# Kernel tuning notes

Measured on AMD Instinct MI355X. Metric: run time of the kernel, lower is better.

## Reference

```python
import jax, jax.numpy as jnp
import numpy as np

EPS = 1e-6

def _rmsnorm(x, w):
    # x: [..., Dh]
    inv = jax.lax.rsqrt(jnp.mean(x * x, axis=-1, keepdims=True) + EPS)
    return x * inv * w

def _apply_rope(x, rope):
    # x: [B, H, L, Dh], rope: [L, Dh//2, 2]
    L = x.shape[-2]
    cos = rope[:L, :, 0]  # [L, Dh//2]
    sin = rope[:L, :, 1]
    x_even = x[..., 0::2]
    x_odd = x[..., 1::2]
    rot = jnp.stack([x_even * cos - x_odd * sin,
                     x_even * sin + x_odd * cos], axis=-1)  # [B,H,L,Dh//2,2]
    return rot.reshape(*x.shape[:-1], -1)


def setup_inputs() -> dict:
    key = jax.random.key(0)
    ks = jax.random.split(key, 4)
    B, L, D = 2, 2048, 1024
    H, Dh = 16, 64
    x = jax.random.normal(ks[0], (B, L, D), dtype=jnp.float32)
    rope = jax.random.normal(ks[1], (L, Dh // 2, 2), dtype=jnp.float32)
    w_qkv = jax.random.normal(ks[2], (3 * D, D), dtype=jnp.float32) * (1.0 / np.sqrt(D))
    w_proj = jax.random.normal(ks[3], (D, D), dtype=jnp.float32) * (1.0 / np.sqrt(D))
    q_norm_w = jnp.ones((Dh,), dtype=jnp.float32)
    k_norm_w = jnp.ones((Dh,), dtype=jnp.float32)
    return {"x": x, "rope": rope, "w_qkv": w_qkv, "w_proj": w_proj,
            "q_norm_w": q_norm_w, "k_norm_w": k_norm_w}


def reference(x, rope, w_qkv, w_proj, q_norm_w, k_norm_w):
    B, L, D = x.shape
    H = 16
    Dh = D // H
    qkv = jnp.einsum('bld,ed->ble', x, w_qkv).reshape(B, L, 3, H, Dh)
    qkv = jnp.transpose(qkv, (2, 0, 3, 1, 4))  # [3, B, H, L, Dh]
    q, k, v = qkv[0], qkv[1], qkv[2]
    q = _rmsnorm(q, q_norm_w)
    k = _rmsnorm(k, k_norm_w)
    q = _apply_rope(q, rope)
    k = _apply_rope(k, rope)
    scale = 1.0 / np.sqrt(Dh)
    scores = jnp.einsum('bhqd,bhkd->bhqk', q, k) * scale
    attn = jax.nn.softmax(scores, axis=-1)
    out = jnp.einsum('bhqk,bhkd->bhqd', attn, v)  # [B,H,L,Dh]
    out = jnp.transpose(out, (0, 2, 1, 3)).reshape(B, L, D)
    return jnp.einsum('bld,ed->ble', out, w_proj)
```

## Files before the change

### kernel.cpp

```cpp
#include <hip/hip_runtime.h>

typedef unsigned short u16;
typedef unsigned int u32;
typedef __bf16 bf16x8 __attribute__((ext_vector_type(8)));
typedef float f32x4 __attribute__((ext_vector_type(4)));

#define L_SEQ 2048
#define NH 16
#define DH 64
#define D_MODEL 1024
#define ATT_SHIFT2 14.426950408889634f

__device__ __forceinline__ u16 f2bf(float f) {
  union { float f; u32 u; } v; v.f = f;
  u32 u = v.u;
  return (u16)((u + 0x7fffu + ((u >> 16) & 1u)) >> 16);
}
__device__ __forceinline__ float bf2f(u16 b) {
  union { u32 u; float f; } v; v.u = ((u32)b) << 16;
  return v.f;
}
__device__ __forceinline__ u32 pk2(float lo_val, float hi_val) {
  union { float f; u32 u; } a, b;
  a.f = hi_val; b.f = lo_val;
  return __builtin_amdgcn_perm(a.u + 0x8000u, b.u + 0x8000u, 0x07060302u);
}
__device__ __forceinline__ u32 pk2t(float lo_val, float hi_val) {
  union { float f; u32 u; } a, b;
  a.f = hi_val; b.f = lo_val;
  return __builtin_amdgcn_perm(a.u, b.u, 0x07060302u);
}
__device__ __forceinline__ bf16x8 ld8(const u16* p) {
  union { uint4 u; bf16x8 b; } v;
  v.u = *(const uint4*)p;
  return v.b;
}
__device__ __forceinline__ f32x4 fzero4() { f32x4 z = {0.f, 0.f, 0.f, 0.f}; return z; }

__device__ __forceinline__ float fexp2(float x) {
#if __has_builtin(__builtin_amdgcn_exp2f)
  return __builtin_amdgcn_exp2f(x);
#else
  return __expf(x * 0.6931471805599453f);
#endif
}

__device__ __forceinline__ void gll16(const u16* g, u16* l) {
  __builtin_amdgcn_global_load_lds((const __attribute__((address_space(1))) u32*)g,
                                   (__attribute__((address_space(3))) u32*)l, 16, 0, 0);
}

__global__ __launch_bounds__(256) void cvt_bf16(const float* __restrict__ src,
                                                u16* __restrict__ dst, int n4) {
  int i = blockIdx.x * 256 + threadIdx.x;
  if (i >= n4) return;
  float4 v = ((const float4*)src)[i];
  ushort4 o = make_ushort4(f2bf(v.x), f2bf(v.y), f2bf(v.z), f2bf(v.w));
  ((ushort4*)dst)[i] = o;
}

template <int BM, bool OUT_BF16>
__global__ __launch_bounds__(256) void gemm_bt(const u16* __restrict__ A,
                                               const u16* __restrict__ B,
                                               void* __restrict__ Cp,
                                               int N, int K) {
  constexpr int MI = BM / 32;
  __shared__ u16 As[BM * 64];
  __shared__ u16 Bs[128 * 64];
  const int t = threadIdx.x;
  const int lane = t & 63, wv = t >> 6;
  const int col = lane & 15, quad = lane >> 4;
  const int wr = wv >> 1, wc = wv & 1;
  const int m0 = blockIdx.y * BM, n0 = blockIdx.x * 128;

  f32x4 acc[MI][4];
#pragma unroll
  for (int i = 0; i < MI; ++i)
#pragma unroll
    for (int j = 0; j < 4; ++j) acc[i][j] = fzero4();

  for (int kt = 0; kt < K; kt += 64) {
    __syncthreads();
#pragma unroll
    for (int it = 0; it < BM / 32; ++it) {
      int id0 = it * 256 + wv * 64;
      int id = id0 + lane;
      int row = id >> 3, cs = id & 7;
      int csrc = cs ^ (row & 7);
      gll16(A + (size_t)(m0 + row) * K + kt + csrc * 8, As + (size_t)id0 * 8);
    }
#pragma unroll
    for (int it = 0; it < 4; ++it) {
      int id0 = it * 256 + wv * 64;
      int id = id0 + lane;
      int row = id >> 3, cs = id & 7;
      int csrc = cs ^ (row & 7);
      gll16(B + (size_t)(n0 + row) * K + kt + csrc * 8, Bs + (size_t)id0 * 8);
    }
    __syncthreads();
#pragma unroll
    for (int c = 0; c < 2; ++c) {
      bf16x8 af[MI], bfv[4];
#pragma unroll
      for (int f = 0; f < MI; ++f) {
        int r = wr * (BM / 2) + f * 16 + col;
        af[f] = ld8(&As[(r * 8 + ((c * 4 + quad) ^ (r & 7))) * 8]);
      }
#pragma unroll
      for (int f = 0; f < 4; ++f) {
        int rb = wc * 64 + f * 16 + col;
        bfv[f] = ld8(&Bs[(rb * 8 + ((c * 4 + quad) ^ (rb & 7))) * 8]);
      }
#pragma unroll
      for (int i = 0; i < MI; ++i)
#pragma unroll
        for (int j = 0; j < 4; ++j)
          acc[i][j] = __builtin_amdgcn_mfma_f32_16x16x32_bf16(af[i], bfv[j], acc[i][j], 0, 0, 0);
    }
  }
#pragma unroll
  for (int i = 0; i < MI; ++i) {
    int gr = m0 + wr * (BM / 2) + i * 16 + quad * 4;
#pragma unroll
    for (int j = 0; j < 4; ++j) {
      int gc = n0 + wc * 64 + j * 16 + col;
#pragma unroll
      for (int r = 0; r < 4; ++r) {
        if (OUT_BF16)
          ((u16*)Cp)[(size_t)(gr + r) * N + gc] = f2bf(acc[i][j][r]);
        else
          ((float*)Cp)[(size_t)(gr + r) * N + gc] = acc[i][j][r];
      }
    }
  }
}

__global__ __launch_bounds__(256) void qk_norm_rope(const u16* __restrict__ qkvb,
                                                    const float* __restrict__ rope,
                                                    const float* __restrict__ qw,
                                                    const float* __restrict__ kw,
                                                    u16* __restrict__ qb,
                                                    u16* __restrict__ kb) {
  const int t = threadIdx.x;
  const int lane = t & 63, wv = t >> 6;
  const int gid = blockIdx.x * 4 + wv;
  const int l = gid & (L_SEQ - 1);
  const int b = gid >> 11;
  const int lg = lane & 7;
  const u16* base = qkvb + (size_t)gid * 3072 + lane * 8;
  const float QSCALE = 0.125f * 1.4426950408889634f;

  float wqv[8], wkv[8], rp[8];
  {
    float4 a = *(const float4*)(qw + lg * 8);
    float4 c = *(const float4*)(qw + lg * 8 + 4);
    wqv[0]=a.x; wqv[1]=a.y; wqv[2]=a.z; wqv[3]=a.w; wqv[4]=c.x; wqv[5]=c.y; wqv[6]=c.z; wqv[7]=c.w;
    a = *(const float4*)(kw + lg * 8);
    c = *(const float4*)(kw + lg * 8 + 4);
    wkv[0]=a.x; wkv[1]=a.y; wkv[2]=a.z; wkv[3]=a.w; wkv[4]=c.x; wkv[5]=c.y; wkv[6]=c.z; wkv[7]=c.w;
    a = *(const float4*)(rope + (size_t)l * 64 + lg * 8);
    c = *(const float4*)(rope + (size_t)l * 64 + lg * 8 + 4);
    rp[0]=a.x; rp[1]=a.y; rp[2]=a.z; rp[3]=a.w; rp[4]=c.x; rp[5]=c.y; rp[6]=c.z; rp[7]=c.w;
  }

#pragma unroll
  for (int i = 0; i < 2; ++i) {
    bf16x8 q8 = ld8(base + i * 512);
    bf16x8 k8 = ld8(base + 1024 + i * 512);
    float q[8], k[8];
#pragma unroll
    for (int j = 0; j < 8; ++j) { q[j] = (float)q8[j]; k[j] = (float)k8[j]; }
    float sq = 0.f, sk = 0.f;
#pragma unroll
    for (int j = 0; j < 8; ++j) { sq += q[j] * q[j]; sk += k[j] * k[j]; }
    sq += __shfl_xor(sq, 1); sq += __shfl_xor(sq, 2); sq += __shfl_xor(sq, 4);
    sk += __shfl_xor(sk, 1); sk += __shfl_xor(sk, 2); sk += __shfl_xor(sk, 4);
    float qi = rsqrtf(sq * (1.f / 64.f) + 1e-6f);
    float ki = rsqrtf(sk * (1.f / 64.f) + 1e-6f);

    float rq[8], rk[8];
#pragma unroll
    for (int j = 0; j < 4; ++j) {
      float cs = rp[2 * j], sn = rp[2 * j + 1];
      float qe = q[2 * j] * qi * wqv[2 * j], qo = q[2 * j + 1] * qi * wqv[2 * j + 1];
      float ke = k[2 * j] * ki * wkv[2 * j], ko = k[2 * j + 1] * ki * wkv[2 * j + 1];
      rq[2 * j]     = (qe * cs - qo * sn) * QSCALE;
      rq[2 * j + 1] = (qe * sn + qo * cs) * QSCALE;
      rk[2 * j]     = ke * cs - ko * sn;
      rk[2 * j + 1] = ke * sn + ko * cs;
    }
    uint4 qp = make_uint4(pk2(rq[0], rq[1]), pk2(rq[2], rq[3]), pk2(rq[4], rq[5]), pk2(rq[6], rq[7]));
    uint4 kp = make_uint4(pk2(rk[0], rk[1]), pk2(rk[2], rk[3]), pk2(rk[4], rk[5]), pk2(rk[6], rk[7]));
    const int head = (lane >> 3) + i * 8;
    size_t oi = (((size_t)(b * NH + head) * L_SEQ + l) * DH) + lg * 8;
    *(uint4*)(qb + oi) = qp;
    *(uint4*)(kb + oi) = kp;
  }
}

__global__ __launch_bounds__(256) void v_transpose(const u16* __restrict__ qkvb,
                                                   u16* __restrict__ vtb) {
  __shared__ u16 ldsT[64 * 64];
  const int t = threadIdx.x;
  const int bid = blockIdx.x;
  const int bh = bid >> 5;
  const int lt = (bid & 31) * 64;
  const int b = bh >> 4, h = bh & 15;
  const u16* src = qkvb + (size_t)(b * L_SEQ + lt) * 3072 + 2048 + h * 64;
#pragma unroll
  for (int i = 0; i < 2; ++i) {
    int idx = i * 256 + t;
    int ll = idx >> 3, dc = idx & 7;
    uint4 v = *(const uint4*)(src + (size_t)ll * 3072 + dc * 8);
    union { uint4 u; u16 s[8]; } vv; vv.u = v;
#pragma unroll
    for (int j = 0; j < 8; ++j) {
      int dh = dc * 8 + j;
      ldsT[dh * 64 + ((((ll >> 3) ^ (dh >> 3)) & 7) * 8 + (ll & 7))] = vv.s[j];
    }
  }
  __syncthreads();
#pragma unroll
  for (int i = 0; i < 2; ++i) {
    int idx = i * 256 + t;
    int dh = idx >> 3, lc = idx & 7;
    uint4 v = *(const uint4*)&ldsT[dh * 64 + (((lc ^ (dh >> 3)) & 7) * 8)];
    *(uint4*)(vtb + ((size_t)bh * 64 + dh) * L_SEQ + lt + lc * 8) = v;
  }
}

__global__ __launch_bounds__(256) void attn_flash(const u16* __restrict__ qb,
                                                  const u16* __restrict__ kb,
                                                  const u16* __restrict__ vtb,
                                                  u16* __restrict__ po,
                                                  float* __restrict__ pl) {
  __shared__ u16 ldsK[2 * 4096];
  __shared__ u16 ldsV[2 * 4096];
  __shared__ u16 ldsP[4 * 1024];
  const int t = threadIdx.x;
  const int lane = t & 63, wv = t >> 6;
  const int col = lane & 15, quad = lane >> 4;
  const int bh = blockIdx.x >> 1;
  const int half = blockIdx.x & 1;
  const int q0 = blockIdx.y * 128 + wv * 32;

  const u16* kbase = kb + ((size_t)bh * L_SEQ + half * 1024) * DH;
  const u16* vbase = vtb + (size_t)bh * DH * L_SEQ + half * 1024;

  bf16x8 qfrag[2][2];
#pragma unroll
  for (int qf = 0; qf < 2; ++qf)
#pragma unroll
    for (int c = 0; c < 2; ++c)
      qfrag[qf][c] = ld8(qb + ((size_t)bh * L_SEQ + q0 + qf * 16 + col) * DH + c * 32 + quad * 8);

  f32x4 o[2][4];
#pragma unroll
  for (int qf = 0; qf < 2; ++qf)
#pragma unroll
    for (int nf = 0; nf < 4; ++nf) o[qf][nf] = fzero4();
  float lrow[2] = {0.f, 0.f};

#pragma unroll
  for (int it = 0; it < 2; ++it) {
    int id0 = it * 256 + wv * 64;
    int id = id0 + lane;
    int row = id >> 3, cs = id & 7, csrc = cs ^ (row & 7);
    gll16(kbase + row * DH + csrc * 8, ldsK + (size_t)id0 * 8);
    gll16(vbase + (size_t)row * L_SEQ + csrc * 8, ldsV + (size_t)id0 * 8);
  }

  u16* pb = &ldsP[wv * 1024];

  for (int tt = 0; tt < 16; ++tt) {
    __syncthreads();
    const int cur = (tt & 1) * 4096;
    if (tt + 1 < 16) {
      const int nxt = ((tt + 1) & 1) * 4096;
      const int kt = (tt + 1) * 64;
#pragma unroll
      for (int it = 0; it < 2; ++it) {
        int id0 = it * 256 + wv * 64;
        int id = id0 + lane;
        int row = id >> 3, cs = id & 7, csrc = cs ^ (row & 7);
        gll16(kbase + (size_t)(kt + row) * DH + csrc * 8, ldsK + nxt + (size_t)id0 * 8);
        gll16(vbase + (size_t)row * L_SEQ + kt + csrc * 8, ldsV + nxt + (size_t)id0 * 8);
      }
    }

    f32x4 s[2][4];
#pragma unroll
    for (int qf = 0; qf < 2; ++qf)
#pragma unroll
      for (int mf = 0; mf < 4; ++mf) s[qf][mf] = fzero4();
#pragma unroll
    for (int c = 0; c < 2; ++c) {
#pragma unroll
      for (int mf = 0; mf < 4; ++mf) {
        int kr = mf * 16 + col;
        bf16x8 kf = ld8(&ldsK[cur + kr * 64 + (((c * 4 + quad) ^ (kr & 7)) * 8)]);
#pragma unroll
        for (int qf = 0; qf < 2; ++qf)
          s[qf][mf] = __builtin_amdgcn_mfma_f32_16x16x32_bf16(kf, qfrag[qf][c], s[qf][mf], 0, 0, 0);
      }
    }

#pragma unroll
    for (int qf = 0; qf < 2; ++qf) {
      float ts = 0.f;
#pragma unroll
      for (int mf = 0; mf < 4; ++mf)
#pragma unroll
        for (int r = 0; r < 4; ++r) {
          float e = fexp2(s[qf][mf][r] - ATT_SHIFT2);
          s[qf][mf][r] = e;
          ts += e;
        }
      lrow[qf] += ts;
#pragma unroll
      for (int mf = 0; mf < 4; ++mf) {
        int slot = col * 8 + (((2 * mf + (quad >> 1))) ^ (col & 7));
        *(uint2*)(pb + slot * 8 + (quad & 1) * 4) =
            make_uint2(pk2t(s[qf][mf][0], s[qf][mf][1]), pk2t(s[qf][mf][2], s[qf][mf][3]));
      }
#pragma unroll
      for (int c = 0; c < 2; ++c) {
        bf16x8 pa = ld8(pb + (col * 8 + ((c * 4 + quad) ^ (col & 7))) * 8);
#pragma unroll
        for (int nf = 0; nf < 4; ++nf) {
          int vr = nf * 16 + col;
          bf16x8 vf = ld8(&ldsV[cur + vr * 64 + (((c * 4 + quad) ^ (vr & 7)) * 8)]);
          o[qf][nf] = __builtin_amdgcn_mfma_f32_16x16x32_bf16(pa, vf, o[qf][nf], 0, 0, 0);
        }
      }
    }
  }

  u16* pob = po + (size_t)(half * 32 + bh) * L_SEQ * DH;
#pragma unroll
  for (int qf = 0; qf < 2; ++qf) {
    lrow[qf] += __shfl_xor(lrow[qf], 16);
    lrow[qf] += __shfl_xor(lrow[qf], 32);
    if (quad == 0)
      pl[(size_t)(half * 32 + bh) * L_SEQ + q0 + qf * 16 + col] = lrow[qf];
#pragma unroll
    for (int nf = 0; nf < 4; ++nf)
#pragma unroll
      for (int r = 0; r < 4; ++r)
        pob[(size_t)(q0 + qf * 16 + quad * 4 + r) * DH + nf * 16 + col] = f2bf(o[qf][nf][r]);
  }
}

__global__ __launch_bounds__(256) void gemm2_cmb(const u16* __restrict__ po,
                                                 const float* __restrict__ pl,
                                                 const u16* __restrict__ B,
                                                 float* __restrict__ out) {
  __shared__ u16 As[64 * 64];
  __shared__ u16 Bs[128 * 64];
  const int t = threadIdx.x;
  const int lane = t & 63, wv = t >> 6;
  const int col = lane & 15, quad = lane >> 4;
  const int wr = wv >> 1, wc = wv & 1;
  const int m0 = blockIdx.y * 64, n0 = blockIdx.x * 128;
  const int srow = t >> 2, kc0 = (t & 3) * 2;
  const int m = m0 + srow, bb = m >> 11, ll = m & 2047;

  f32x4 acc[2][4];
#pragma unroll
  for (int i = 0; i < 2; ++i)
#pragma unroll
    for (int j = 0; j < 4; ++j) acc[i][j] = fzero4();

  for (int kt = 0; kt < 1024; kt += 64) {
    __syncthreads();
    {
      int h = kt >> 6;
      size_t lidx = (size_t)(bb * 16 + h) * L_SEQ + ll;
      float inv = 1.0f / (pl[lidx] + pl[65536 + lidx]);
      size_t rowoff = lidx * 64;
#pragma unroll
      for (int i = 0; i < 2; ++i) {
        int kc = kc0 + i;
        uint4 a0 = *(const uint4*)(po + rowoff + kc * 8);
        uint4 a1 = *(const uint4*)(po + 4194304 + rowoff + kc * 8);
        union { uint4 u; u16 s[8]; } ua, ub;
        ua.u = a0; ub.u = a1;
        float r[8];
#pragma unroll
        for (int j = 0; j < 8; ++j) r[j] = (bf2f(ua.s[j]) + bf2f(ub.s[j])) * inv;
        uint4 pk = make_uint4(pk2(r[0], r[1]), pk2(r[2], r[3]), pk2(r[4], r[5]), pk2(r[6], r[7]));
        int slot = srow * 8 + (kc ^ (srow & 7));
        *(uint4*)(As + slot * 8) = pk;
      }
    }
#pragma unroll
    for (int it = 0; it < 4; ++it) {
      int id0 = it * 256 + wv * 64;
      int id = id0 + lane;
      int row = id >> 3, cs = id & 7, csrc = cs ^ (row & 7);
      gll16(B + (size_t)(n0 + row) * 1024 + kt + csrc * 8, Bs + (size_t)id0 * 8);
    }
    __syncthreads();
#pragma unroll
    for (int c = 0; c < 2; ++c) {
      bf16x8 af[2], bfv[4];
#pragma unroll
      for (int f = 0; f < 2; ++f) {
        int r = wr * 32 + f * 16 + col;
        af[f] = ld8(&As[(r * 8 + ((c * 4 + quad) ^ (r & 7))) * 8]);
      }
#pragma unroll
      for (int f = 0; f < 4; ++f) {
        int rb = wc * 64 + f * 16 + col;
        bfv[f] = ld8(&Bs[(rb * 8 + ((c * 4 + quad) ^ (rb & 7))) * 8]);
      }
#pragma unroll
      for (int i = 0; i < 2; ++i)
#pragma unroll
        for (int j = 0; j < 4; ++j)
          acc[i][j] = __builtin_amdgcn_mfma_f32_16x16x32_bf16(af[i], bfv[j], acc[i][j], 0, 0, 0);
    }
  }
#pragma unroll
  for (int i = 0; i < 2; ++i) {
    int gr = m0 + wr * 32 + i * 16 + quad * 4;
#pragma unroll
    for (int j = 0; j < 4; ++j) {
      int gc = n0 + wc * 64 + j * 16 + col;
#pragma unroll
      for (int r = 0; r < 4; ++r)
        out[(size_t)(gr + r) * D_MODEL + gc] = acc[i][j][r];
    }
  }
}

extern "C" void kernel_launch(void* const* d_in, const int* in_sizes, int n_in,
                              void* d_out, int out_size, void* d_ws, size_t ws_size,
                              hipStream_t stream) {
  const float* x     = (const float*)d_in[0];
  const float* rope  = (const float*)d_in[1];
  const float* wqkv  = (const float*)d_in[2];
  const float* wproj = (const float*)d_in[3];
  const float* qnw   = (const float*)d_in[4];
  const float* knw   = (const float*)d_in[5];
  float* out = (float*)d_out;
  char* ws = (char*)d_ws;

  u16* xb     = (u16*)(ws + 0);
  u16* wqkvb  = (u16*)(ws + 8388608);
  u16* wprojb = (u16*)(ws + 14680064);
  u16* qkvb   = (u16*)(ws + 16777216);
  u16* qb     = (u16*)(ws + 41943040);
  u16* kb     = (u16*)(ws + 50331648);
  u16* vtb    = (u16*)(ws + 58720256);
  u16* po     = qkvb;
  float* pl   = (float*)(ws + 33554432);

  cvt_bf16<<<4096, 256, 0, stream>>>(x, xb, 1048576);
  cvt_bf16<<<3072, 256, 0, stream>>>(wqkv, wqkvb, 786432);
  cvt_bf16<<<1024, 256, 0, stream>>>(wproj, wprojb, 262144);

  gemm_bt<128, true><<<dim3(24, 32), 256, 0, stream>>>(xb, wqkvb, (void*)qkvb, 3072, 1024);

  qk_norm_rope<<<1024, 256, 0, stream>>>(qkvb, rope, qnw, knw, qb, kb);
  v_transpose<<<1024, 256, 0, stream>>>(qkvb, vtb);

  attn_flash<<<dim3(64, 16), 256, 0, stream>>>(qb, kb, vtb, po, pl);

  gemm2_cmb<<<dim3(8, 64), 256, 0, stream>>>(po, pl, wprojb, out);
}
```

Baseline: 212.4 us.

## Fuse QKV GEMM epilogue with head scatter and V transpose, merge conversions

Merges the three fp32-to-bf16 conversion launches into one kernel. The QKV GEMM now writes Q and K straight into the per-head layout and transposes V through LDS inside its epilogue, which removes the intermediate qkv buffer and the separate v_transpose kernel. Norm and RoPE now run in place on the head-layout buffers. The attention kernel drops K/V double buffering for a single buffer with an extra barrier, changes its grid mapping to a z-dimension split, and reorders the PV MFMAs so each V fragment is reused across both query fragments. This cuts launches and memory traffic, but the attention loop can no longer overlap loads with compute.

```diff
diff --git a/kernel.cpp b/kernel.cpp
--- a/kernel.cpp
+++ b/kernel.cpp
@@ -50,104 +50,129 @@
                                    (__attribute__((address_space(3))) u32*)l, 16, 0, 0);
 }
 
-__global__ __launch_bounds__(256) void cvt_bf16(const float* __restrict__ src,
-                                                u16* __restrict__ dst, int n4) {
+__global__ __launch_bounds__(256) void cvt_all(const float* __restrict__ x,
+                                               const float* __restrict__ wqkv,
+                                               const float* __restrict__ wproj,
+                                               u16* __restrict__ xb,
+                                               u16* __restrict__ wqkvb,
+                                               u16* __restrict__ wprojb) {
   int i = blockIdx.x * 256 + threadIdx.x;
-  if (i >= n4) return;
-  float4 v = ((const float4*)src)[i];
-  ushort4 o = make_ushort4(f2bf(v.x), f2bf(v.y), f2bf(v.z), f2bf(v.w));
-  ((ushort4*)dst)[i] = o;
-}
-
-template <int BM, bool OUT_BF16>
-__global__ __launch_bounds__(256) void gemm_bt(const u16* __restrict__ A,
-                                               const u16* __restrict__ B,
-                                               void* __restrict__ Cp,
-                                               int N, int K) {
-  constexpr int MI = BM / 32;
-  __shared__ u16 As[BM * 64];
-  __shared__ u16 Bs[128 * 64];
+  const float* s;
+  u16* d;
+  int off;
+  if (i < 1048576)      { s = x;     d = xb;     off = i; }
+  else if (i < 1835008) { s = wqkv;  d = wqkvb;  off = i - 1048576; }
+  else                  { s = wproj; d = wprojb; off = i - 1835008; }
+  float4 v = ((const float4*)s)[off];
+  ((ushort4*)d)[off] = make_ushort4(f2bf(v.x), f2bf(v.y), f2bf(v.z), f2bf(v.w));
+}
+
+__global__ __launch_bounds__(256) void gemm_qkv(const u16* __restrict__ A,
+                                                const u16* __restrict__ B,
+                                                u16* __restrict__ qb,
+                                                u16* __restrict__ kb,
+                                                u16* __restrict__ vtb) {
+  __shared__ u16 smem[16384];
+  u16* As = smem;
+  u16* Bs = smem + 8192;
   const int t = threadIdx.x;
   const int lane = t & 63, wv = t >> 6;
   const int col = lane & 15, quad = lane >> 4;
   const int wr = wv >> 1, wc = wv & 1;
-  const int m0 = blockIdx.y * BM, n0 = blockIdx.x * 128;
-
-  f32x4 acc[MI][4];
-#pragma unroll
-  for (int i = 0; i < MI; ++i)
+  const int m0 = blockIdx.y * 128, n0 = blockIdx.x * 128;
+
+  f32x4 acc[4][4];
+#pragma unroll
+  for (int i = 0; i < 4; ++i)
 #pragma unroll
     for (int j = 0; j < 4; ++j) acc[i][j] = fzero4();
 
-  for (int kt = 0; kt < K; kt += 64) {
-    __syncthreads();
-#pragma unroll
-    for (int it = 0; it < BM / 32; ++it) {
-      int id0 = it * 256 + wv * 64;
-      int id = id0 + lane;
-      int row = id >> 3, cs = id & 7;
-      int csrc = cs ^ (row & 7);
-      gll16(A + (size_t)(m0 + row) * K + kt + csrc * 8, As + (size_t)id0 * 8);
-    }
+  for (int kt = 0; kt < 1024; kt += 64) {
+    __syncthreads();
 #pragma unroll
     for (int it = 0; it < 4; ++it) {
       int id0 = it * 256 + wv * 64;
       int id = id0 + lane;
       int row = id >> 3, cs = id & 7;
       int csrc = cs ^ (row & 7);
-      gll16(B + (size_t)(n0 + row) * K + kt + csrc * 8, Bs + (size_t)id0 * 8);
+      gll16(A + (size_t)(m0 + row) * 1024 + kt + csrc * 8, As + (size_t)id0 * 8);
+      gll16(B + (size_t)(n0 + row) * 1024 + kt + csrc * 8, Bs + (size_t)id0 * 8);
     }
     __syncthreads();
 #pragma unroll
     for (int c = 0; c < 2; ++c) {
-      bf16x8 af[MI], bfv[4];
-#pragma unroll
-      for (int f = 0; f < MI; ++f) {
-        int r = wr * (BM / 2) + f * 16 + col;
+      bf16x8 af[4], bfv[4];
+#pragma unroll
+      for (int f = 0; f < 4; ++f) {
+        int r = wr * 64 + f * 16 + col;
         af[f] = ld8(&As[(r * 8 + ((c * 4 + quad) ^ (r & 7))) * 8]);
-      }
-#pragma unroll
-      for (int f = 0; f < 4; ++f) {
         int rb = wc * 64 + f * 16 + col;
         bfv[f] = ld8(&Bs[(rb * 8 + ((c * 4 + quad) ^ (rb & 7))) * 8]);
       }
 #pragma unroll
-      for (int i = 0; i < MI; ++i)
+      for (int i = 0; i < 4; ++i)
 #pragma unroll
         for (int j = 0; j < 4; ++j)
           acc[i][j] = __builtin_amdgcn_mfma_f32_16x16x32_bf16(af[i], bfv[j], acc[i][j], 0, 0, 0);
     }
   }
-#pragma unroll
-  for (int i = 0; i < MI; ++i) {
-    int gr = m0 + wr * (BM / 2) + i * 16 + quad * 4;
-#pragma unroll
-    for (int j = 0; j < 4; ++j) {
-      int gc = n0 + wc * 64 + j * 16 + col;
-#pragma unroll
-      for (int r = 0; r < 4; ++r) {
-        if (OUT_BF16)
-          ((u16*)Cp)[(size_t)(gr + r) * N + gc] = f2bf(acc[i][j][r]);
-        else
-          ((float*)Cp)[(size_t)(gr + r) * N + gc] = acc[i][j][r];
-      }
-    }
-  }
-}
-
-__global__ __launch_bounds__(256) void qk_norm_rope(const u16* __restrict__ qkvb,
+
+  const int region = n0 >> 10;
+  if (region < 2) {
+    u16* dst = region ? kb : qb;
+#pragma unroll
+    for (int i = 0; i < 4; ++i) {
+      int gr = m0 + wr * 64 + i * 16 + quad * 4;
+      int b = gr >> 11, l = gr & 2047;
+#pragma unroll
+      for (int j = 0; j < 4; ++j) {
+        int gc = (n0 & 1023) + wc * 64 + j * 16 + col;
+        int h = gc >> 6, dh = gc & 63;
+        size_t base = ((size_t)(b * NH + h) * L_SEQ + l) * DH + dh;
+#pragma unroll
+        for (int r = 0; r < 4; ++r)
+          dst[base + (size_t)r * DH] = f2bf(acc[i][j][r]);
+      }
+    }
+  } else {
+    __syncthreads();
+#pragma unroll
+    for (int i = 0; i < 4; ++i) {
+      int m_l = wr * 64 + i * 16 + quad * 4;
+#pragma unroll
+      for (int j = 0; j < 4; ++j) {
+        int n_l = wc * 64 + j * 16 + col;
+        int ta = n_l * 128 + (m_l ^ ((n_l & 15) << 3));
+        *(uint2*)(smem + ta) = make_uint2(pk2(acc[i][j][0], acc[i][j][1]),
+                                          pk2(acc[i][j][2], acc[i][j][3]));
+      }
+    }
+    __syncthreads();
+    const int b = m0 >> 11, lbase = m0 & 2047;
+    const int n_l = t >> 1, mh = (t & 1) * 64;
+    const int gc = (n0 - 2048) + n_l;
+    const int h = gc >> 6, dh = gc & 63;
+    u16* vrow = vtb + ((size_t)(b * NH + h) * DH + dh) * L_SEQ + lbase + mh;
+#pragma unroll
+    for (int c2 = 0; c2 < 8; ++c2) {
+      int m = mh + c2 * 8;
+      uint4 v = *(const uint4*)(smem + n_l * 128 + (m ^ ((n_l & 15) << 3)));
+      *(uint4*)(vrow + c2 * 8) = v;
+    }
+  }
+}
+
+__global__ __launch_bounds__(256) void qk_norm_rope(u16* __restrict__ qb,
+                                                    u16* __restrict__ kb,
                                                     const float* __restrict__ rope,
                                                     const float* __restrict__ qw,
-                                                    const float* __restrict__ kw,
-                                                    u16* __restrict__ qb,
-                                                    u16* __restrict__ kb) {
+                                                    const float* __restrict__ kw) {
   const int t = threadIdx.x;
   const int lane = t & 63, wv = t >> 6;
   const int gid = blockIdx.x * 4 + wv;
   const int l = gid & (L_SEQ - 1);
   const int b = gid >> 11;
   const int lg = lane & 7;
-  const u16* base = qkvb + (size_t)gid * 3072 + lane * 8;
   const float QSCALE = 0.125f * 1.4426950408889634f;
 
   float wqv[8], wkv[8], rp[8];
@@ -165,8 +190,10 @@
 
 #pragma unroll
   for (int i = 0; i < 2; ++i) {
-    bf16x8 q8 = ld8(base + i * 512);
-    bf16x8 k8 = ld8(base + 1024 + i * 512);
+    const int head = i * 8 + (lane >> 3);
+    size_t addr = ((size_t)(b * NH + head) * L_SEQ + l) * DH + lg * 8;
+    bf16x8 q8 = ld8(qb + addr);
+    bf16x8 k8 = ld8(kb + addr);
     float q[8], k[8];
 #pragma unroll
     for (int j = 0; j < 8; ++j) { q[j] = (float)q8[j]; k[j] = (float)k8[j]; }
@@ -189,43 +216,10 @@
       rk[2 * j]     = ke * cs - ko * sn;
       rk[2 * j + 1] = ke * sn + ko * cs;
     }
-    uint4 qp = make_uint4(pk2(rq[0], rq[1]), pk2(rq[2], rq[3]), pk2(rq[4], rq[5]), pk2(rq[6], rq[7]));
-    uint4 kp = make_uint4(pk2(rk[0], rk[1]), pk2(rk[2], rk[3]), pk2(rk[4], rk[5]), pk2(rk[6], rk[7]));
-    const int head = (lane >> 3) + i * 8;
-    size_t oi = (((size_t)(b * NH + head) * L_SEQ + l) * DH) + lg * 8;
-    *(uint4*)(qb + oi) = qp;
-    *(uint4*)(kb + oi) = kp;
-  }
-}
-
-__global__ __launch_bounds__(256) void v_transpose(const u16* __restrict__ qkvb,
-                                                   u16* __restrict__ vtb) {
-  __shared__ u16 ldsT[64 * 64];
-  const int t = threadIdx.x;
-  const int bid = blockIdx.x;
-  const int bh = bid >> 5;
-  const int lt = (bid & 31) * 64;
-  const int b = bh >> 4, h = bh & 15;
-  const u16* src = qkvb + (size_t)(b * L_SEQ + lt) * 3072 + 2048 + h * 64;
-#pragma unroll
-  for (int i = 0; i < 2; ++i) {
-    int idx = i * 256 + t;
-    int ll = idx >> 3, dc = idx & 7;
-    uint4 v = *(const uint4*)(src + (size_t)ll * 3072 + dc * 8);
-    union { uint4 u; u16 s[8]; } vv; vv.u = v;
-#pragma unroll
-    for (int j = 0; j < 8; ++j) {
-      int dh = dc * 8 + j;
-      ldsT[dh * 64 + ((((ll >> 3) ^ (dh >> 3)) & 7) * 8 + (ll & 7))] = vv.s[j];
-    }
-  }
-  __syncthreads();
-#pragma unroll
-  for (int i = 0; i < 2; ++i) {
-    int idx = i * 256 + t;
-    int dh = idx >> 3, lc = idx & 7;
-    uint4 v = *(const uint4*)&ldsT[dh * 64 + (((lc ^ (dh >> 3)) & 7) * 8)];
-    *(uint4*)(vtb + ((size_t)bh * 64 + dh) * L_SEQ + lt + lc * 8) = v;
+    *(uint4*)(qb + addr) = make_uint4(pk2(rq[0], rq[1]), pk2(rq[2], rq[3]),
+                                      pk2(rq[4], rq[5]), pk2(rq[6], rq[7]));
+    *(uint4*)(kb + addr) = make_uint4(pk2(rk[0], rk[1]), pk2(rk[2], rk[3]),
+                                      pk2(rk[4], rk[5]), pk2(rk[6], rk[7]));
   }
 }
 
@@ -234,14 +228,14 @@
                                                   const u16* __restrict__ vtb,
                                                   u16* __restrict__ po,
                                                   float* __restrict__ pl) {
-  __shared__ u16 ldsK[2 * 4096];
-  __shared__ u16 ldsV[2 * 4096];
-  __shared__ u16 ldsP[4 * 1024];
+  __shared__ u16 ldsK[4096];
+  __shared__ u16 ldsV[4096];
+  __shared__ u16 ldsP[8192];
   const int t = threadIdx.x;
   const int lane = t & 63, wv = t >> 6;
   const int col = lane & 15, quad = lane >> 4;
-  const int bh = blockIdx.x >> 1;
-  const int half = blockIdx.x & 1;
+  const int bh = blockIdx.x;
+  const int half = blockIdx.z;
   const int q0 = blockIdx.y * 128 + wv * 32;
 
   const u16* kbase = kb + ((size_t)bh * L_SEQ + half * 1024) * DH;
@@ -261,32 +255,22 @@
     for (int nf = 0; nf < 4; ++nf) o[qf][nf] = fzero4();
   float lrow[2] = {0.f, 0.f};
 
-#pragma unroll
-  for (int it = 0; it < 2; ++it) {
-    int id0 = it * 256 + wv * 64;
-    int id = id0 + lane;
-    int row = id >> 3, cs = id & 7, csrc = cs ^ (row & 7);
-    gll16(kbase + row * DH + csrc * 8, ldsK + (size_t)id0 * 8);
-    gll16(vbase + (size_t)row * L_SEQ + csrc * 8, ldsV + (size_t)id0 * 8);
-  }
-
-  u16* pb = &ldsP[wv * 1024];
+  u16* pb = &ldsP[wv * 2048];
 
   for (int tt = 0; tt < 16; ++tt) {
     __syncthreads();
-    const int cur = (tt & 1) * 4096;
-    if (tt + 1 < 16) {
-      const int nxt = ((tt + 1) & 1) * 4096;
-      const int kt = (tt + 1) * 64;
+    {
+      const int kt = tt * 64;
 #pragma unroll
       for (int it = 0; it < 2; ++it) {
         int id0 = it * 256 + wv * 64;
         int id = id0 + lane;
         int row = id >> 3, cs = id & 7, csrc = cs ^ (row & 7);
-        gll16(kbase + (size_t)(kt + row) * DH + csrc * 8, ldsK + nxt + (size_t)id0 * 8);
-        gll16(vbase + (size_t)row * L_SEQ + kt + csrc * 8, ldsV + nxt + (size_t)id0 * 8);
-      }
-    }
+        gll16(kbase + (size_t)(kt + row) * DH + csrc * 8, ldsK + (size_t)id0 * 8);
+        gll16(vbase + (size_t)row * L_SEQ + kt + csrc * 8, ldsV + (size_t)id0 * 8);
+      }
+    }
+    __syncthreads();
 
     f32x4 s[2][4];
 #pragma unroll
@@ -298,7 +282,7 @@
 #pragma unroll
       for (int mf = 0; mf < 4; ++mf) {
         int kr = mf * 16 + col;
-        bf16x8 kf = ld8(&ldsK[cur + kr * 64 + (((c * 4 + quad) ^ (kr & 7)) * 8)]);
+        bf16x8 kf = ld8(&ldsK[kr * 64 + (((c * 4 + quad) ^ (kr & 7)) * 8)]);
 #pragma unroll
         for (int qf = 0; qf < 2; ++qf)
           s[qf][mf] = __builtin_amdgcn_mfma_f32_16x16x32_bf16(kf, qfrag[qf][c], s[qf][mf], 0, 0, 0);
@@ -317,21 +301,30 @@
           ts += e;
         }
       lrow[qf] += ts;
+      const int q = qf * 16 + col;
 #pragma unroll
       for (int mf = 0; mf < 4; ++mf) {
-        int slot = col * 8 + (((2 * mf + (quad >> 1))) ^ (col & 7));
+        int slot = q * 8 + ((2 * mf + (quad >> 1)) ^ (q & 7));
         *(uint2*)(pb + slot * 8 + (quad & 1) * 4) =
             make_uint2(pk2t(s[qf][mf][0], s[qf][mf][1]), pk2t(s[qf][mf][2], s[qf][mf][3]));
       }
-#pragma unroll
-      for (int c = 0; c < 2; ++c) {
-        bf16x8 pa = ld8(pb + (col * 8 + ((c * 4 + quad) ^ (col & 7))) * 8);
-#pragma unroll
-        for (int nf = 0; nf < 4; ++nf) {
-          int vr = nf * 16 + col;
-          bf16x8 vf = ld8(&ldsV[cur + vr * 64 + (((c * 4 + quad) ^ (vr & 7)) * 8)]);
-          o[qf][nf] = __builtin_amdgcn_mfma_f32_16x16x32_bf16(pa, vf, o[qf][nf], 0, 0, 0);
-        }
+    }
+
+#pragma unroll
+    for (int c = 0; c < 2; ++c) {
+      bf16x8 pa[2];
+#pragma unroll
+      for (int qf = 0; qf < 2; ++qf) {
+        const int q = qf * 16 + col;
+        pa[qf] = ld8(pb + (q * 8 + ((c * 4 + quad) ^ (q & 7))) * 8);
+      }
+#pragma unroll
+      for (int nf = 0; nf < 4; ++nf) {
+        int vr = nf * 16 + col;
+        bf16x8 vf = ld8(&ldsV[vr * 64 + (((c * 4 + quad) ^ (vr & 7)) * 8)]);
+#pragma unroll
+        for (int qf = 0; qf < 2; ++qf)
+          o[qf][nf] = __builtin_amdgcn_mfma_f32_16x16x32_bf16(pa[qf], vf, o[qf][nf], 0, 0, 0);
       }
     }
   }
@@ -449,23 +442,19 @@
   u16* xb     = (u16*)(ws + 0);
   u16* wqkvb  = (u16*)(ws + 8388608);
   u16* wprojb = (u16*)(ws + 14680064);
-  u16* qkvb   = (u16*)(ws + 16777216);
-  u16* qb     = (u16*)(ws + 41943040);
-  u16* kb     = (u16*)(ws + 50331648);
-  u16* vtb    = (u16*)(ws + 58720256);
-  u16* po     = qkvb;
-  float* pl   = (float*)(ws + 33554432);
-
-  cvt_bf16<<<4096, 256, 0, stream>>>(x, xb, 1048576);
-  cvt_bf16<<<3072, 256, 0, stream>>>(wqkv, wqkvb, 786432);
-  cvt_bf16<<<1024, 256, 0, stream>>>(wproj, wprojb, 262144);
-
-  gemm_bt<128, true><<<dim3(24, 32), 256, 0, stream>>>(xb, wqkvb, (void*)qkvb, 3072, 1024);
-
-  qk_norm_rope<<<1024, 256, 0, stream>>>(qkvb, rope, qnw, knw, qb, kb);
-  v_transpose<<<1024, 256, 0, stream>>>(qkvb, vtb);
-
-  attn_flash<<<dim3(64, 16), 256, 0, stream>>>(qb, kb, vtb, po, pl);
+  u16* qb     = (u16*)(ws + 16777216);
+  u16* kb     = (u16*)(ws + 25165824);
+  u16* vtb    = (u16*)(ws + 33554432);
+  u16* po     = (u16*)(ws + 41943040);
+  float* pl   = (float*)(ws + 58720256);
+
+  cvt_all<<<8192, 256, 0, stream>>>(x, wqkv, wproj, xb, wqkvb, wprojb);
+
+  gemm_qkv<<<dim3(24, 32), 256, 0, stream>>>(xb, wqkvb, qb, kb, vtb);
+
+  qk_norm_rope<<<1024, 256, 0, stream>>>(qb, kb, rope, qnw, knw);
+
+  attn_flash<<<dim3(32, 16, 2), 256, 0, stream>>>(qb, kb, vtb, po, pl);
 
   gemm2_cmb<<<dim3(8, 64), 256, 0, stream>>>(po, pl, wprojb, out);
 }
```

New measurement: 214.9 us. Within noise of the previous version (+1.2%).
